# Optimization experiments

Hardware: AMD Instinct MI355X
Metric: run time of the kernel (lower is better)

## Reference

```python
import jax, jax.numpy as jnp
import numpy as np
import math

IN_DIM = 1024
OUT_DIM = 1024
GRID_SIZE = 5
SPLINE_ORDER = 3
N_COEFFS = GRID_SIZE + SPLINE_ORDER          # 8
N_KNOTS = GRID_SIZE + 2 * SPLINE_ORDER + 1   # 12
EPS = 1e-08


def setup_inputs() -> dict:
    key = jax.random.key(0)
    k_x, k_c, k_w = jax.random.split(key, 3)
    B = 4096
    x = jax.random.normal(k_x, (B, IN_DIM), dtype=jnp.float32)
    coeffs = jax.random.normal(k_c, (OUT_DIM, IN_DIM * N_COEFFS), dtype=jnp.float32) * 0.1
    # kaiming_uniform(a=sqrt(5)) -> U(-bound, bound), bound = sqrt(6/((1+a^2)*fan_in)) = 1/sqrt(fan_in)
    bound = 1.0 / math.sqrt(IN_DIM)
    base_weight = jax.random.uniform(k_w, (OUT_DIM, IN_DIM), dtype=jnp.float32,
                                     minval=-bound, maxval=bound)
    step = 2.0 / GRID_SIZE
    init_val = math.log(math.exp(step) - 1.0)
    grid_steps_log = jnp.full((IN_DIM, N_KNOTS - 1), init_val, dtype=jnp.float32)
    grid_start = jnp.full((IN_DIM, 1), -1.0 - SPLINE_ORDER * step, dtype=jnp.float32)
    res_scale = jnp.zeros((1,), dtype=jnp.float32)
    return {"x": x, "coeffs": coeffs, "base_weight": base_weight,
            "grid_steps_log": grid_steps_log, "grid_start": grid_start,
            "res_scale": res_scale}


def _get_grid(grid_steps_log, grid_start):
    steps = jax.nn.softplus(grid_steps_log)            # [in, n_knots-1]
    grid = jnp.concatenate([grid_start, steps], axis=-1)
    return jnp.cumsum(grid, axis=-1)                   # [in, n_knots]


def _b_spline(x, grid):
    # x: [B, in], grid: [in, n_knots] -> bases: [B, in, n_coeffs]
    x_u = x[:, :, None]                                # [B, in, 1]
    g = grid[None, :, :]                               # [1, in, n_knots]
    bases = ((x_u >= g[:, :, :-1]) & (x_u < g[:, :, 1:])).astype(x.dtype)
    for d in range(1, SPLINE_ORDER + 1):
        left = (x_u - g[:, :, :-(d + 1)]) / (g[:, :, d:-1] - g[:, :, :-(d + 1)] + EPS)
        right = (g[:, :, d + 1:] - x_u) / (g[:, :, d + 1:] - g[:, :, 1:-d] + EPS)
        bases = left * bases[:, :, :-1] + right * bases[:, :, 1:]
    return bases


def reference(x, coeffs, base_weight, grid_steps_log, grid_start, res_scale):
    grid = _get_grid(grid_steps_log, grid_start)
    spline_basis = _b_spline(x, grid)                  # [B, in, n_coeffs]
    B = spline_basis.shape[0]
    spline_flat = spline_basis.reshape(B, -1)          # [B, in*n_coeffs]
    spline_out = spline_flat @ coeffs.T                # [B, out]
    base_out = jax.nn.silu(x) @ base_weight.T          # [B, out]
    y = spline_out + base_out
    y = y + res_scale * x                              # residual (in_dim == out_dim)
    return y
```

## Files before the change

kernel.cpp:

```cpp
#include <hip/hip_runtime.h>

#define IN_DIM   1024
#define OUT_DIM  1024
#define BATCH    4096
#define NC       8
#define NK       12
#define KSPLINE  (IN_DIM * NC)
#define KDIM     (KSPLINE + IN_DIM)
#define EPS      1e-8f

#define NBLK_A   ((IN_DIM / 256) * (BATCH / 16))
#define NBLK_W   ((OUT_DIM * (KDIM / 4)) / 256)

#define KSPLIT   4
#define BKQ      32
#define KPS      (KDIM / KSPLIT)
#define NKT      (KPS / BKQ)
#define NGBLK    ((BATCH / 256) * (OUT_DIM / 256) * KSPLIT)

typedef _Float16 f16x8  __attribute__((ext_vector_type(8)));
typedef float    f32x4  __attribute__((ext_vector_type(4)));

static __device__ __forceinline__ unsigned short f2h_bits(float f) {
  _Float16 h = (_Float16)f;
  return __builtin_bit_cast(unsigned short, h);
}

static __device__ __forceinline__ void gl_lds16(const unsigned short* g, unsigned short* l) {
  __builtin_amdgcn_global_load_lds(
      (const __attribute__((address_space(1))) unsigned int*)g,
      (__attribute__((address_space(3))) unsigned int*)l, 16, 0, 0);
}

__global__ __launch_bounds__(256) void prep_k(const float* __restrict__ x,
                                              const float* __restrict__ coeffs,
                                              const float* __restrict__ bw,
                                              const float* __restrict__ gsl,
                                              const float* __restrict__ gstart,
                                              const float* __restrict__ rsp,
                                              unsigned short* __restrict__ A,
                                              unsigned short* __restrict__ W,
                                              float* __restrict__ out) {
  const int blk = blockIdx.x;
  if (blk < NBLK_A) {
    const int i  = (blk & 3) * 256 + threadIdx.x;
    const int b0 = (blk >> 2) * 16;
    const float rs = rsp[0];
    float g[NK];
    float acc = gstart[i];
    g[0] = acc;
#pragma unroll
    for (int t = 0; t < NK - 1; ++t) {
      float v  = gsl[i * (NK - 1) + t];
      float sp = (v > 20.f) ? v : log1pf(expf(v));
      acc += sp;
      g[t + 1] = acc;
    }
    float r[30];
#pragma unroll
    for (int j = 0; j < 11; ++j) r[j]      = 1.f / (g[j + 1] - g[j] + EPS);
#pragma unroll
    for (int j = 0; j < 10; ++j) r[11 + j] = 1.f / (g[j + 2] - g[j] + EPS);
#pragma unroll
    for (int j = 0; j <  9; ++j) r[21 + j] = 1.f / (g[j + 3] - g[j] + EPS);

    for (int bb = 0; bb < 16; ++bb) {
      const int b = b0 + bb;
      float xv = x[(size_t)b * IN_DIM + i];
      float bas[NK - 1];
#pragma unroll
      for (int k = 0; k < NK - 1; ++k)
        bas[k] = (xv >= g[k] && xv < g[k + 1]) ? 1.f : 0.f;
      const int off[3] = {0, 11, 21};
#pragma unroll
      for (int d = 1; d <= 3; ++d) {
#pragma unroll
        for (int k = 0; k < NK - 1 - d; ++k) {
          float left  = (xv - g[k])         * r[off[d - 1] + k];
          float right = (g[k + d + 1] - xv) * r[off[d - 1] + k + 1];
          bas[k] = left * bas[k] + right * bas[k + 1];
        }
      }
      uint4 pack;
      pack.x = (unsigned)f2h_bits(bas[0]) | ((unsigned)f2h_bits(bas[1]) << 16);
      pack.y = (unsigned)f2h_bits(bas[2]) | ((unsigned)f2h_bits(bas[3]) << 16);
      pack.z = (unsigned)f2h_bits(bas[4]) | ((unsigned)f2h_bits(bas[5]) << 16);
      pack.w = (unsigned)f2h_bits(bas[6]) | ((unsigned)f2h_bits(bas[7]) << 16);
      *(uint4*)&A[(size_t)b * KDIM + i * NC] = pack;
      float s = xv / (1.f + expf(-xv));
      A[(size_t)b * KDIM + KSPLINE + i] = f2h_bits(s);
      out[(size_t)b * OUT_DIM + i] = rs * xv;
    }
  } else {
    int idx = (blk - NBLK_A) * 256 + threadIdx.x;
    int n  = idx / (KDIM / 4);
    int k4 = (idx - n * (KDIM / 4)) * 4;
    float4 v;
    if (k4 < KSPLINE) v = *(const float4*)&coeffs[(size_t)n * KSPLINE + k4];
    else              v = *(const float4*)&bw[(size_t)n * IN_DIM + (k4 - KSPLINE)];
    ushort4 o;
    o.x = f2h_bits(v.x); o.y = f2h_bits(v.y); o.z = f2h_bits(v.z); o.w = f2h_bits(v.w);
    *(ushort4*)&W[(size_t)n * KDIM + k4] = o;
  }
}

__global__ __launch_bounds__(512, 2) void gemm_k(const unsigned short* __restrict__ A,
                                                 const unsigned short* __restrict__ W,
                                                 float* __restrict__ out) {
  __shared__ __align__(16) unsigned short As[4][256][BKQ];
  __shared__ __align__(16) unsigned short Bs[4][256][BKQ];
  const int tid  = threadIdx.x;
  const int wave = tid >> 6;
  const int lane = tid & 63;

  const int s  = (blockIdx.x & 7) * 32 + (blockIdx.x >> 3);
  const int ks = s >> 6;
  const int bn = (s >> 4) & 3;
  const int bm = s & 15;

  const int srow = tid >> 2;
  const int scsw = ((tid & 3) ^ (srow & 3)) * 8;
  const unsigned short* aG = A + (size_t)(bm * 256 + srow) * KDIM + (size_t)ks * KPS + scsw;
  const unsigned short* bG = W + (size_t)(bn * 256 + srow) * KDIM + (size_t)ks * KPS + scsw;

#define STAGE(t) do {                                                          \
    const int sl_ = (t) & 3; const int kb_ = (t) * BKQ;                        \
    gl_lds16(aG + kb_,                      &As[sl_][wave * 16][0]);           \
    gl_lds16(aG + (size_t)128 * KDIM + kb_, &As[sl_][128 + wave * 16][0]);     \
    gl_lds16(bG + kb_,                      &Bs[sl_][wave * 16][0]);           \
    gl_lds16(bG + (size_t)128 * KDIM + kb_, &Bs[sl_][128 + wave * 16][0]);     \
  } while (0)

  const int l15 = lane & 15;
  const int kg  = lane >> 4;
  const int wm  = (wave >> 2) * 128;
  const int wn  = (wave & 3) * 64;

  f32x4 acc[8][4] = {};

  STAGE(0); STAGE(1); STAGE(2);
  asm volatile("s_waitcnt vmcnt(8)" ::: "memory");
  __builtin_amdgcn_s_barrier();

#pragma unroll 4
  for (int kt = 0; kt < NKT; ++kt) {
    if (kt < NKT - 3) STAGE(kt + 3);
    const unsigned short* as = &As[kt & 3][0][0];
    const unsigned short* bs = &Bs[kt & 3][0][0];
    f16x8 af[8], bf[4];
#pragma unroll
    for (int nt = 0; nt < 4; ++nt) {
      int row = wn + nt * 16 + l15;
      bf[nt] = *(const f16x8*)&bs[row * BKQ + ((kg ^ (row & 3)) * 8)];
    }
#pragma unroll
    for (int mt = 0; mt < 8; ++mt) {
      int row = wm + mt * 16 + l15;
      af[mt] = *(const f16x8*)&as[row * BKQ + ((kg ^ (row & 3)) * 8)];
    }
    __builtin_amdgcn_s_setprio(1);
#pragma unroll
    for (int mt = 0; mt < 8; ++mt)
#pragma unroll
      for (int nt = 0; nt < 4; ++nt)
        acc[mt][nt] = __builtin_amdgcn_mfma_f32_16x16x32_f16(af[mt], bf[nt], acc[mt][nt], 0, 0, 0);
    __builtin_amdgcn_s_setprio(0);
    if (kt < NKT - 3)       asm volatile("s_waitcnt vmcnt(8)" ::: "memory");
    else if (kt == NKT - 3) asm volatile("s_waitcnt vmcnt(4)" ::: "memory");
    else if (kt == NKT - 2) asm volatile("s_waitcnt vmcnt(0)" ::: "memory");
    if (kt < NKT - 1) __builtin_amdgcn_s_barrier();
  }
#undef STAGE

#pragma unroll
  for (int mt = 0; mt < 8; ++mt) {
#pragma unroll
    for (int reg = 0; reg < 4; ++reg) {
      const int row = bm * 256 + wm + mt * 16 + kg * 4 + reg;
      float* orow = out + (size_t)row * OUT_DIM;
#pragma unroll
      for (int nt = 0; nt < 4; ++nt) {
        const int col = bn * 256 + wn + nt * 16 + l15;
        atomicAdd(&orow[col], acc[mt][nt][reg]);
      }
    }
  }
}

extern "C" void kernel_launch(void* const* d_in, const int* in_sizes, int n_in,
                              void* d_out, int out_size, void* d_ws, size_t ws_size,
                              hipStream_t stream) {
  const float* x      = (const float*)d_in[0];
  const float* coeffs = (const float*)d_in[1];
  const float* bw     = (const float*)d_in[2];
  const float* gsl    = (const float*)d_in[3];
  const float* gstart = (const float*)d_in[4];
  const float* rsp    = (const float*)d_in[5];

  char* ws = (char*)d_ws;
  unsigned short* A  = (unsigned short*)ws;
  unsigned short* W  = (unsigned short*)(ws + (size_t)BATCH * KDIM * 2);
  float*          out = (float*)d_out;

  prep_k<<<NBLK_A + NBLK_W, 256, 0, stream>>>(x, coeffs, bw, gsl, gstart, rsp, A, W, out);
  gemm_k<<<NGBLK, 512, 0, stream>>>(A, W, out);
}
```

Measured before the change: 253.3 us.

## Split GEMM k-step into two half-phases interleaving LDS reads, loads, and MFMAs

Each k-tile iteration of the GEMM main loop is split into two halves. Each half reads half of the A fragments from LDS, issues half of the global-to-LDS prefetch (A then B), and runs its MFMAs, with extra barriers added between phases. The LDS XOR swizzle changes from row&3 to (row>>1)&3 to alter the bank-conflict pattern for the 16-byte reads. The aim is to overlap memory issue with matrix math and reduce register pressure, at the cost of three extra workgroup barriers per iteration.

```diff
diff --git a/kernel.cpp b/kernel.cpp
--- a/kernel.cpp
+++ b/kernel.cpp
@@ -17,6 +17,8 @@
 #define KPS      (KDIM / KSPLIT)
 #define NKT      (KPS / BKQ)
 #define NGBLK    ((BATCH / 256) * (OUT_DIM / 256) * KSPLIT)
+
+#define SWZ(r)   (((r) >> 1) & 3)
 
 typedef _Float16 f16x8  __attribute__((ext_vector_type(8)));
 typedef float    f32x4  __attribute__((ext_vector_type(4)));
@@ -119,14 +121,17 @@
   const int bm = s & 15;
 
   const int srow = tid >> 2;
-  const int scsw = ((tid & 3) ^ (srow & 3)) * 8;
+  const int scsw = ((tid & 3) ^ SWZ(srow)) * 8;
   const unsigned short* aG = A + (size_t)(bm * 256 + srow) * KDIM + (size_t)ks * KPS + scsw;
   const unsigned short* bG = W + (size_t)(bn * 256 + srow) * KDIM + (size_t)ks * KPS + scsw;
 
-#define STAGE(t) do {                                                          \
+#define STAGE_A(t) do {                                                        \
     const int sl_ = (t) & 3; const int kb_ = (t) * BKQ;                        \
     gl_lds16(aG + kb_,                      &As[sl_][wave * 16][0]);           \
     gl_lds16(aG + (size_t)128 * KDIM + kb_, &As[sl_][128 + wave * 16][0]);     \
+  } while (0)
+#define STAGE_B(t) do {                                                        \
+    const int sl_ = (t) & 3; const int kb_ = (t) * BKQ;                        \
     gl_lds16(bG + kb_,                      &Bs[sl_][wave * 16][0]);           \
     gl_lds16(bG + (size_t)128 * KDIM + kb_, &Bs[sl_][128 + wave * 16][0]);     \
   } while (0)
@@ -138,39 +143,58 @@
 
   f32x4 acc[8][4] = {};
 
-  STAGE(0); STAGE(1); STAGE(2);
+  STAGE_A(0); STAGE_B(0); STAGE_A(1); STAGE_B(1); STAGE_A(2); STAGE_B(2);
   asm volatile("s_waitcnt vmcnt(8)" ::: "memory");
   __builtin_amdgcn_s_barrier();
 
 #pragma unroll 4
   for (int kt = 0; kt < NKT; ++kt) {
-    if (kt < NKT - 3) STAGE(kt + 3);
     const unsigned short* as = &As[kt & 3][0][0];
     const unsigned short* bs = &Bs[kt & 3][0][0];
-    f16x8 af[8], bf[4];
+    f16x8 af[4], bf[4];
+
+#pragma unroll
+    for (int mt = 0; mt < 4; ++mt) {
+      int row = wm + mt * 16 + l15;
+      af[mt] = *(const f16x8*)&as[row * BKQ + ((kg ^ SWZ(row)) * 8)];
+    }
 #pragma unroll
     for (int nt = 0; nt < 4; ++nt) {
       int row = wn + nt * 16 + l15;
-      bf[nt] = *(const f16x8*)&bs[row * BKQ + ((kg ^ (row & 3)) * 8)];
-    }
-#pragma unroll
-    for (int mt = 0; mt < 8; ++mt) {
-      int row = wm + mt * 16 + l15;
-      af[mt] = *(const f16x8*)&as[row * BKQ + ((kg ^ (row & 3)) * 8)];
-    }
+      bf[nt] = *(const f16x8*)&bs[row * BKQ + ((kg ^ SWZ(row)) * 8)];
+    }
+    if (kt < NKT - 3) STAGE_A(kt + 3);
+    __builtin_amdgcn_s_barrier();
     __builtin_amdgcn_s_setprio(1);
 #pragma unroll
-    for (int mt = 0; mt < 8; ++mt)
+    for (int mt = 0; mt < 4; ++mt)
 #pragma unroll
       for (int nt = 0; nt < 4; ++nt)
         acc[mt][nt] = __builtin_amdgcn_mfma_f32_16x16x32_f16(af[mt], bf[nt], acc[mt][nt], 0, 0, 0);
+    __builtin_amdgcn_s_setprio(0);
+    __builtin_amdgcn_s_barrier();
+
+#pragma unroll
+    for (int mt = 0; mt < 4; ++mt) {
+      int row = wm + 64 + mt * 16 + l15;
+      af[mt] = *(const f16x8*)&as[row * BKQ + ((kg ^ SWZ(row)) * 8)];
+    }
+    if (kt < NKT - 3) STAGE_B(kt + 3);
+    __builtin_amdgcn_s_barrier();
+    __builtin_amdgcn_s_setprio(1);
+#pragma unroll
+    for (int mt = 0; mt < 4; ++mt)
+#pragma unroll
+      for (int nt = 0; nt < 4; ++nt)
+        acc[4 + mt][nt] = __builtin_amdgcn_mfma_f32_16x16x32_f16(af[mt], bf[nt], acc[4 + mt][nt], 0, 0, 0);
     __builtin_amdgcn_s_setprio(0);
     if (kt < NKT - 3)       asm volatile("s_waitcnt vmcnt(8)" ::: "memory");
     else if (kt == NKT - 3) asm volatile("s_waitcnt vmcnt(4)" ::: "memory");
     else if (kt == NKT - 2) asm volatile("s_waitcnt vmcnt(0)" ::: "memory");
     if (kt < NKT - 1) __builtin_amdgcn_s_barrier();
   }
-#undef STAGE
+#undef STAGE_A
+#undef STAGE_B
 
 #pragma unroll
   for (int mt = 0; mt < 8; ++mt) {
```

Result: no change. 248.3 us (-2.0%).

## Replace split-K 256x256 GEMM tiles with 128x64 tiles and non-atomic stores

Applied to the files above, without the earlier changes.

Drops the four-way K split and uses smaller 128x64 output tiles with 256-thread blocks. Each block now owns its output tile, so atomic adds become plain read-modify-write. The swizzle pattern changes, and global-to-LDS prefetch is moved after the LDS fragment reads. This trades the atomic and split-K overhead for lower data reuse per tile and more LDS traffic per MFMA.

```diff
diff --git a/kernel.cpp b/kernel.cpp
--- a/kernel.cpp
+++ b/kernel.cpp
@@ -12,11 +12,13 @@
 #define NBLK_A   ((IN_DIM / 256) * (BATCH / 16))
 #define NBLK_W   ((OUT_DIM * (KDIM / 4)) / 256)
 
-#define KSPLIT   4
+#define BM       128
+#define BN       64
 #define BKQ      32
-#define KPS      (KDIM / KSPLIT)
-#define NKT      (KPS / BKQ)
-#define NGBLK    ((BATCH / 256) * (OUT_DIM / 256) * KSPLIT)
+#define NKT      (KDIM / BKQ)
+#define NGBLK    ((BATCH / BM) * (OUT_DIM / BN))
+
+#define SWZ(r)   (((r) >> 1) & 3)
 
 typedef _Float16 f16x8  __attribute__((ext_vector_type(8)));
 typedef float    f32x4  __attribute__((ext_vector_type(4)));
@@ -104,84 +106,84 @@
   }
 }
 
-__global__ __launch_bounds__(512, 2) void gemm_k(const unsigned short* __restrict__ A,
+__global__ __launch_bounds__(256, 2) void gemm_k(const unsigned short* __restrict__ A,
                                                  const unsigned short* __restrict__ W,
                                                  float* __restrict__ out) {
-  __shared__ __align__(16) unsigned short As[4][256][BKQ];
-  __shared__ __align__(16) unsigned short Bs[4][256][BKQ];
+  __shared__ __align__(16) unsigned short As[4][BM][BKQ];
+  __shared__ __align__(16) unsigned short Bs[4][BN][BKQ];
   const int tid  = threadIdx.x;
   const int wave = tid >> 6;
   const int lane = tid & 63;
 
-  const int s  = (blockIdx.x & 7) * 32 + (blockIdx.x >> 3);
-  const int ks = s >> 6;
-  const int bn = (s >> 4) & 3;
-  const int bm = s & 15;
-
-  const int srow = tid >> 2;
-  const int scsw = ((tid & 3) ^ (srow & 3)) * 8;
-  const unsigned short* aG = A + (size_t)(bm * 256 + srow) * KDIM + (size_t)ks * KPS + scsw;
-  const unsigned short* bG = W + (size_t)(bn * 256 + srow) * KDIM + (size_t)ks * KPS + scsw;
+  const int xcd = blockIdx.x & 7;
+  const int idx = blockIdx.x >> 3;
+  const int bm  = xcd * 4 + (idx & 3);
+  const int bn  = idx >> 2;
+
+  const int srow = wave * 16 + (lane >> 2);
+  const int scsw = ((lane & 3) ^ SWZ(srow)) * 8;
+  const unsigned short* aG = A + (size_t)(bm * BM + srow) * KDIM + scsw;
+  const unsigned short* bG = W + (size_t)(bn * BN + srow) * KDIM + scsw;
 
 #define STAGE(t) do {                                                          \
     const int sl_ = (t) & 3; const int kb_ = (t) * BKQ;                        \
-    gl_lds16(aG + kb_,                      &As[sl_][wave * 16][0]);           \
-    gl_lds16(aG + (size_t)128 * KDIM + kb_, &As[sl_][128 + wave * 16][0]);     \
-    gl_lds16(bG + kb_,                      &Bs[sl_][wave * 16][0]);           \
-    gl_lds16(bG + (size_t)128 * KDIM + kb_, &Bs[sl_][128 + wave * 16][0]);     \
+    gl_lds16(aG + kb_,                     &As[sl_][wave * 16][0]);            \
+    gl_lds16(aG + (size_t)64 * KDIM + kb_, &As[sl_][64 + wave * 16][0]);       \
+    gl_lds16(bG + kb_,                     &Bs[sl_][wave * 16][0]);            \
   } while (0)
 
   const int l15 = lane & 15;
   const int kg  = lane >> 4;
-  const int wm  = (wave >> 2) * 128;
-  const int wn  = (wave & 3) * 64;
-
-  f32x4 acc[8][4] = {};
+  const int wm  = (wave >> 1) * 64;
+  const int wn  = (wave & 1) * 32;
+
+  f32x4 acc[4][2] = {};
 
   STAGE(0); STAGE(1); STAGE(2);
-  asm volatile("s_waitcnt vmcnt(8)" ::: "memory");
+  asm volatile("s_waitcnt vmcnt(6)" ::: "memory");
   __builtin_amdgcn_s_barrier();
 
 #pragma unroll 4
   for (int kt = 0; kt < NKT; ++kt) {
-    if (kt < NKT - 3) STAGE(kt + 3);
     const unsigned short* as = &As[kt & 3][0][0];
     const unsigned short* bs = &Bs[kt & 3][0][0];
-    f16x8 af[8], bf[4];
-#pragma unroll
-    for (int nt = 0; nt < 4; ++nt) {
+    f16x8 af[4], bf[2];
+#pragma unroll
+    for (int mt = 0; mt < 4; ++mt) {
+      int row = wm + mt * 16 + l15;
+      af[mt] = *(const f16x8*)&as[row * BKQ + ((kg ^ SWZ(row)) * 8)];
+    }
+#pragma unroll
+    for (int nt = 0; nt < 2; ++nt) {
       int row = wn + nt * 16 + l15;
-      bf[nt] = *(const f16x8*)&bs[row * BKQ + ((kg ^ (row & 3)) * 8)];
-    }
-#pragma unroll
-    for (int mt = 0; mt < 8; ++mt) {
-      int row = wm + mt * 16 + l15;
-      af[mt] = *(const f16x8*)&as[row * BKQ + ((kg ^ (row & 3)) * 8)];
-    }
+      bf[nt] = *(const f16x8*)&bs[row * BKQ + ((kg ^ SWZ(row)) * 8)];
+    }
+    if (kt < NKT - 3) STAGE(kt + 3);
+    __builtin_amdgcn_sched_barrier(0);
     __builtin_amdgcn_s_setprio(1);
 #pragma unroll
-    for (int mt = 0; mt < 8; ++mt)
-#pragma unroll
-      for (int nt = 0; nt < 4; ++nt)
+    for (int mt = 0; mt < 4; ++mt)
+#pragma unroll
+      for (int nt = 0; nt < 2; ++nt)
         acc[mt][nt] = __builtin_amdgcn_mfma_f32_16x16x32_f16(af[mt], bf[nt], acc[mt][nt], 0, 0, 0);
     __builtin_amdgcn_s_setprio(0);
-    if (kt < NKT - 3)       asm volatile("s_waitcnt vmcnt(8)" ::: "memory");
-    else if (kt == NKT - 3) asm volatile("s_waitcnt vmcnt(4)" ::: "memory");
+    if (kt < NKT - 3)       asm volatile("s_waitcnt vmcnt(6)" ::: "memory");
+    else if (kt == NKT - 3) asm volatile("s_waitcnt vmcnt(3)" ::: "memory");
     else if (kt == NKT - 2) asm volatile("s_waitcnt vmcnt(0)" ::: "memory");
     if (kt < NKT - 1) __builtin_amdgcn_s_barrier();
   }
 #undef STAGE
 
 #pragma unroll
-  for (int mt = 0; mt < 8; ++mt) {
+  for (int mt = 0; mt < 4; ++mt) {
 #pragma unroll
     for (int reg = 0; reg < 4; ++reg) {
-      const int row = bm * 256 + wm + mt * 16 + kg * 4 + reg;
+      const int row = bm * BM + wm + mt * 16 + kg * 4 + reg;
       float* orow = out + (size_t)row * OUT_DIM;
 #pragma unroll
-      for (int nt = 0; nt < 4; ++nt) {
-        const int col = bn * 256 + wn + nt * 16 + l15;
-        atomicAdd(&orow[col], acc[mt][nt][reg]);
+      for (int nt = 0; nt < 2; ++nt) {
+        const int col = bn * BN + wn + nt * 16 + l15;
+        orow[col] += acc[mt][nt][reg];
       }
     }
   }
@@ -203,5 +205,5 @@
   float*          out = (float*)d_out;
 
   prep_k<<<NBLK_A + NBLK_W, 256, 0, stream>>>(x, coeffs, bw, gsl, gstart, rsp, A, W, out);
-  gemm_k<<<NGBLK, 512, 0, stream>>>(A, W, out);
-}
+  gemm_k<<<NGBLK, 256, 0, stream>>>(A, W, out);
+}
```

Result: faster. 247.5 us (-2.3%).
